# Kernel optimization log

Measured on AMD Instinct MI355X. Metric: run time of the kernel, lower is better.

## Reference

```python
import jax, jax.numpy as jnp
import numpy as np

N_HEAD = 16
N_STATE = 1024
NEG_INF = -1e9


def setup_inputs() -> dict:
    key = jax.random.key(0)
    k1, = jax.random.split(key, 1)
    B, S = 4, 2048
    x = jax.random.normal(k1, (B, S, 3 * N_STATE), dtype=jnp.float32)
    # causal attention mask (1 = keep, 0 = masked), broadcast over heads
    attn_mask = jnp.tril(jnp.ones((S, S), dtype=jnp.float32))[None, None, :, :]
    attn_mask = jnp.broadcast_to(attn_mask, (B, 1, S, S))
    return {"x": x, "attn_mask": attn_mask}


def reference(x, attn_mask) -> jnp.ndarray:
    B, S, _ = x.shape
    d_head = N_STATE // N_HEAD
    q = x[:, :, :N_STATE].reshape(B, S, N_HEAD, d_head).transpose(0, 2, 1, 3)  # [B,H,S,D]
    k = x[:, :, N_STATE:2 * N_STATE].reshape(B, S, N_HEAD, d_head).transpose(0, 2, 1, 3)
    v = x[:, :, 2 * N_STATE:].reshape(B, S, N_HEAD, d_head).transpose(0, 2, 1, 3)
    scale = 1.0 / jnp.sqrt(jnp.asarray(d_head, dtype=x.dtype))
    w = jnp.einsum('bhqd,bhkd->bhqk', q, k) * scale           # [B,H,S,S]
    w = attn_mask * w + (1.0 - attn_mask) * NEG_INF
    w = jax.nn.softmax(w, axis=-1)
    # attention_dropout is identity at inference (Keras Dropout, training=False)
    a = jnp.einsum('bhqk,bhkd->bhqd', w, v)                   # [B,H,S,D]
    return a.transpose(0, 2, 1, 3).reshape(B, S, N_STATE)
```

## Files before the change

kernel.cpp:

```cpp
#include <hip/hip_runtime.h>


typedef float  f32x4  __attribute__((ext_vector_type(4)));
typedef short  bf16x8 __attribute__((ext_vector_type(8)));

#define NH      16
#define DH      64
#define SEQ     2048
#define NSTATE  1024
#define ROW3    3072
#define BQ      128
#define BK      64
#define NQB     (SEQ / BQ)
#define KST     72
#define VST     72
#define PST     72
#define NEG_BIG (-1e9f)
#define QSC     (0.125f * 1.4426950408889634f)

static __device__ __forceinline__ unsigned pk2(float x, float y) {
    unsigned ux = __builtin_bit_cast(unsigned, x);
    unsigned uy = __builtin_bit_cast(unsigned, y);
    ux += 0x7FFFu + ((ux >> 16) & 1u);
    uy += 0x7FFFu + ((uy >> 16) & 1u);
    return __builtin_amdgcn_perm(uy, ux, 0x07060302u);
}

__global__ __launch_bounds__(512, 4)
void mha_fwd(const float* __restrict__ x, float* __restrict__ out) {
    const int tid  = threadIdx.x;
    const int wave = tid >> 6;
    const int lane = tid & 63;
    const int l16  = lane & 15;
    const int quad = lane >> 4;

    const int pr = blockIdx.x;
    const int bh = blockIdx.y;
    const int b  = bh >> 4;
    const int h  = bh & 15;

    const float* xb    = x + (size_t)b * SEQ * ROW3;
    const float* kbase = xb + NSTATE + h * DH;
    const float* vbase = xb + 2 * NSTATE + h * DH;
    float*       ob    = out + (size_t)b * SEQ * NSTATE + h * DH;

    __shared__ __align__(16) short Klds[BK * KST];
    __shared__ __align__(16) short Vlds[DH * VST];
    __shared__ __align__(16) short Plds[8][16 * PST];

    bf16x8 vones;
#pragma unroll
    for (int i = 0; i < 8; ++i) vones[i] = (short)0x3F80;

#pragma unroll 1
    for (int ph = 0; ph < 2; ++ph) {
        const int qblk = ph ? (NQB - 1 - pr) : pr;
        const int q0   = qblk * BQ;
        const int qmin = q0 + wave * 16;
        const int qrow = qmin + l16;

        bf16x8 qf[2];
        {
            const float* qp = xb + (size_t)qrow * ROW3 + h * DH + quad * 8;
#pragma unroll
            for (int f = 0; f < 2; ++f) {
                float4 a = *(const float4*)(qp + 32 * f);
                float4 c = *(const float4*)(qp + 32 * f + 4);
                union { bf16x8 v; unsigned u[4]; } qq;
                qq.u[0] = pk2(a.x * QSC, a.y * QSC);
                qq.u[1] = pk2(a.z * QSC, a.w * QSC);
                qq.u[2] = pk2(c.x * QSC, c.y * QSC);
                qq.u[3] = pk2(c.z * QSC, c.w * QSC);
                qf[f] = qq.v;
            }
        }

        f32x4 o[4];
#pragma unroll
        for (int t = 0; t < 4; ++t) o[t] = (f32x4){0.f, 0.f, 0.f, 0.f};
        f32x4 ol = (f32x4){0.f, 0.f, 0.f, 0.f};

        const int ntiles = q0 / BK + BQ / BK;
#pragma unroll 1
        for (int it = 0; it < ntiles; ++it) {
            const int kv0 = it * BK;
            __syncthreads();

#pragma unroll
            for (int i = 0; i < 2; ++i) {
                int p  = tid + 512 * i;
                int kv = p >> 4;
                int d  = (p & 15) * 4;
                const float* gp = kbase + (size_t)(kv0 + kv) * ROW3 + d;
                float4 v = *(const float4*)gp;
                uint2 pk;
                pk.x = pk2(v.x, v.y);
                pk.y = pk2(v.z, v.w);
                *(uint2*)&Klds[kv * KST + d] = pk;
            }
#pragma unroll
            for (int i = 0; i < 4; ++i) {
                int idx = tid + 512 * i;
                int d   = idx & 63;
                int kv  = (idx >> 6) * 2;
                const float* gp = vbase + (size_t)(kv0 + kv) * ROW3 + d;
                float v0 = gp[0];
                float v1 = gp[ROW3];
                *(unsigned*)&Vlds[d * VST + kv] = pk2(v0, v1);
            }
            __syncthreads();

            if (kv0 > qmin + 15) continue;

            bf16x8 kf[4][2];
#pragma unroll
            for (int t = 0; t < 4; ++t)
#pragma unroll
                for (int f = 0; f < 2; ++f)
                    kf[t][f] = *(const bf16x8*)&Klds[(16 * t + l16) * KST + quad * 8 + 32 * f];
            bf16x8 vf[4][2];
#pragma unroll
            for (int t = 0; t < 4; ++t)
#pragma unroll
                for (int f = 0; f < 2; ++f)
                    vf[t][f] = *(const bf16x8*)&Vlds[(16 * t + l16) * VST + quad * 8 + 32 * f];

            f32x4 sc[4];
#pragma unroll
            for (int t = 0; t < 4; ++t) {
                f32x4 c = (f32x4){0.f, 0.f, 0.f, 0.f};
                c = __builtin_amdgcn_mfma_f32_16x16x32_bf16(kf[t][0], qf[0], c, 0, 0, 0);
                c = __builtin_amdgcn_mfma_f32_16x16x32_bf16(kf[t][1], qf[1], c, 0, 0, 0);
                sc[t] = c;
            }
            if (kv0 + BK - 1 > qmin) {
#pragma unroll
                for (int t = 0; t < 4; ++t)
#pragma unroll
                    for (int r = 0; r < 4; ++r) {
                        int kvg = kv0 + 16 * t + 4 * quad + r;
                        if (kvg > qrow) sc[t][r] = NEG_BIG;
                    }
            }

#pragma unroll
            for (int t = 0; t < 4; ++t)
#pragma unroll
                for (int r = 0; r < 4; ++r)
                    sc[t][r] = __builtin_amdgcn_exp2f(sc[t][r]);

            short* pb = &Plds[wave][0];
#pragma unroll
            for (int t = 0; t < 4; ++t) {
                uint2 pk;
                pk.x = pk2(sc[t][0], sc[t][1]);
                pk.y = pk2(sc[t][2], sc[t][3]);
                *(uint2*)&pb[l16 * PST + 16 * t + 4 * quad] = pk;
            }
            __asm__ volatile("s_waitcnt lgkmcnt(0)" ::: "memory");
            bf16x8 pf0 = *(const bf16x8*)&pb[l16 * PST + quad * 8];
            bf16x8 pf1 = *(const bf16x8*)&pb[l16 * PST + quad * 8 + 32];

#pragma unroll
            for (int t = 0; t < 4; ++t) {
                f32x4 c = o[t];
                c = __builtin_amdgcn_mfma_f32_16x16x32_bf16(pf0, vf[t][0], c, 0, 0, 0);
                c = __builtin_amdgcn_mfma_f32_16x16x32_bf16(pf1, vf[t][1], c, 0, 0, 0);
                o[t] = c;
            }
            ol = __builtin_amdgcn_mfma_f32_16x16x32_bf16(pf0, vones, ol, 0, 0, 0);
            ol = __builtin_amdgcn_mfma_f32_16x16x32_bf16(pf1, vones, ol, 0, 0, 0);
        }

        {
            const int qtop = qmin + 4 * quad;
            float lr[4];
#pragma unroll
            for (int r = 0; r < 4; ++r) lr[r] = 1.0f / ol[r];
#pragma unroll
            for (int t = 0; t < 4; ++t)
#pragma unroll
                for (int r = 0; r < 4; ++r)
                    ob[(size_t)(qtop + r) * NSTATE + 16 * t + l16] = o[t][r] * lr[r];
        }
    }
}

extern "C" void kernel_launch(void* const* d_in, const int* in_sizes, int n_in,
                              void* d_out, int out_size, void* d_ws, size_t ws_size,
                              hipStream_t stream) {
    const float* x = (const float*)d_in[0];
    float* out = (float*)d_out;
    dim3 grid(NQB / 2, 4 * NH);
    dim3 block(512);
    hipLaunchKernelGGL(mha_fwd, grid, block, 0, stream, x, out);
}
```

Baseline: 254.6 us.

## Fuse paired query blocks into one KV sweep with double-buffered LDS prefetch

Instead of two sequential phases that each reload K/V tiles, the block processes its low and high query blocks together in a single sweep over KV tiles, sharing each loaded K/V tile between both. The global loads for the next tile are issued into registers before computing on the current tile and committed to a second LDS buffer afterwards, which drops one barrier per iteration and hides load latency. In exchange it needs more registers (two sets of accumulators and Q fragments plus prefetch registers) and doubles K/V LDS use, which may reduce occupancy.

After: 629.9 us. +147.4%, slower.

```diff
diff --git a/kernel.cpp b/kernel.cpp
--- a/kernel.cpp
+++ b/kernel.cpp
@@ -26,6 +26,127 @@
     return __builtin_amdgcn_perm(uy, ux, 0x07060302u);
 }
 
+#define ISSUE_STAGE(KV0)                                                       \
+    {                                                                          \
+        _Pragma("unroll")                                                      \
+        for (int i = 0; i < 2; ++i) {                                          \
+            int p  = tid + 512 * i;                                            \
+            int kv = p >> 4;                                                   \
+            int d  = (p & 15) * 4;                                             \
+            kp[i] = *(const float4*)(kbase + (size_t)((KV0) + kv) * ROW3 + d); \
+        }                                                                      \
+        _Pragma("unroll")                                                      \
+        for (int i = 0; i < 4; ++i) {                                          \
+            int idx = tid + 512 * i;                                           \
+            int d   = idx & 63;                                                \
+            int kv  = (idx >> 6) * 2;                                          \
+            const float* gp = vbase + (size_t)((KV0) + kv) * ROW3 + d;         \
+            vp[2 * i]     = gp[0];                                             \
+            vp[2 * i + 1] = gp[ROW3];                                          \
+        }                                                                      \
+    }
+
+#define COMMIT_STAGE(BUF)                                                      \
+    {                                                                          \
+        _Pragma("unroll")                                                      \
+        for (int i = 0; i < 2; ++i) {                                          \
+            int p  = tid + 512 * i;                                            \
+            int kv = p >> 4;                                                   \
+            int d  = (p & 15) * 4;                                             \
+            uint2 w;                                                           \
+            w.x = pk2(kp[i].x, kp[i].y);                                       \
+            w.y = pk2(kp[i].z, kp[i].w);                                       \
+            *(uint2*)&Klds[BUF][kv * KST + d] = w;                             \
+        }                                                                      \
+        _Pragma("unroll")                                                      \
+        for (int i = 0; i < 4; ++i) {                                          \
+            int idx = tid + 512 * i;                                           \
+            int d   = idx & 63;                                                \
+            int kv  = (idx >> 6) * 2;                                          \
+            *(unsigned*)&Vlds[BUF][d * VST + kv] = pk2(vp[2 * i], vp[2 * i + 1]); \
+        }                                                                      \
+    }
+
+#define LOAD_Q(Q0, QF)                                                         \
+    {                                                                          \
+        const int qrow_ = (Q0) + wave * 16 + l16;                              \
+        const float* qp = xb + (size_t)qrow_ * ROW3 + h * DH + quad * 8;       \
+        _Pragma("unroll")                                                      \
+        for (int f = 0; f < 2; ++f) {                                          \
+            float4 a = *(const float4*)(qp + 32 * f);                          \
+            float4 c = *(const float4*)(qp + 32 * f + 4);                      \
+            union { bf16x8 v; unsigned u[4]; } qq;                             \
+            qq.u[0] = pk2(a.x * QSC, a.y * QSC);                               \
+            qq.u[1] = pk2(a.z * QSC, a.w * QSC);                               \
+            qq.u[2] = pk2(c.x * QSC, c.y * QSC);                               \
+            qq.u[3] = pk2(c.z * QSC, c.w * QSC);                               \
+            QF[f] = qq.v;                                                      \
+        }                                                                      \
+    }
+
+#define COMPUTE_BLOCK(Q0, QF, OACC, OL)                                        \
+    {                                                                          \
+        const int qmin_ = (Q0) + wave * 16;                                    \
+        if (kv0 <= qmin_ + 15) {                                               \
+            const int qrow_ = qmin_ + l16;                                     \
+            f32x4 sc[4];                                                       \
+            _Pragma("unroll")                                                  \
+            for (int t = 0; t < 4; ++t) {                                      \
+                f32x4 c = (f32x4){0.f, 0.f, 0.f, 0.f};                         \
+                c = __builtin_amdgcn_mfma_f32_16x16x32_bf16(kf[t][0], QF[0], c, 0, 0, 0); \
+                c = __builtin_amdgcn_mfma_f32_16x16x32_bf16(kf[t][1], QF[1], c, 0, 0, 0); \
+                sc[t] = c;                                                     \
+            }                                                                  \
+            if (kv0 + BK - 1 > qmin_) {                                        \
+                _Pragma("unroll")                                              \
+                for (int t = 0; t < 4; ++t)                                    \
+                    _Pragma("unroll")                                          \
+                    for (int r = 0; r < 4; ++r) {                              \
+                        int kvg = kv0 + 16 * t + 4 * quad + r;                 \
+                        if (kvg > qrow_) sc[t][r] = NEG_BIG;                   \
+                    }                                                          \
+            }                                                                  \
+            _Pragma("unroll")                                                  \
+            for (int t = 0; t < 4; ++t)                                        \
+                _Pragma("unroll")                                              \
+                for (int r = 0; r < 4; ++r)                                    \
+                    sc[t][r] = __builtin_amdgcn_exp2f(sc[t][r]);               \
+            short* pb = &Plds[wave][0];                                        \
+            _Pragma("unroll")                                                  \
+            for (int t = 0; t < 4; ++t) {                                      \
+                uint2 pk;                                                      \
+                pk.x = pk2(sc[t][0], sc[t][1]);                                \
+                pk.y = pk2(sc[t][2], sc[t][3]);                                \
+                *(uint2*)&pb[l16 * PST + 16 * t + 4 * quad] = pk;              \
+            }                                                                  \
+            __asm__ volatile("s_waitcnt lgkmcnt(0)" ::: "memory");             \
+            bf16x8 pf0 = *(const bf16x8*)&pb[l16 * PST + quad * 8];            \
+            bf16x8 pf1 = *(const bf16x8*)&pb[l16 * PST + quad * 8 + 32];       \
+            _Pragma("unroll")                                                  \
+            for (int t = 0; t < 4; ++t) {                                      \
+                f32x4 c = OACC[t];                                             \
+                c = __builtin_amdgcn_mfma_f32_16x16x32_bf16(pf0, vf[t][0], c, 0, 0, 0); \
+                c = __builtin_amdgcn_mfma_f32_16x16x32_bf16(pf1, vf[t][1], c, 0, 0, 0); \
+                OACC[t] = c;                                                   \
+            }                                                                  \
+            OL = __builtin_amdgcn_mfma_f32_16x16x32_bf16(pf0, vones, OL, 0, 0, 0); \
+            OL = __builtin_amdgcn_mfma_f32_16x16x32_bf16(pf1, vones, OL, 0, 0, 0); \
+        }                                                                      \
+    }
+
+#define EPILOGUE(Q0, OACC, OL)                                                 \
+    {                                                                          \
+        const int qtop_ = (Q0) + wave * 16 + 4 * quad;                         \
+        float lr[4];                                                           \
+        _Pragma("unroll")                                                      \
+        for (int r = 0; r < 4; ++r) lr[r] = 1.0f / OL[r];                      \
+        _Pragma("unroll")                                                      \
+        for (int t = 0; t < 4; ++t)                                            \
+            _Pragma("unroll")                                                  \
+            for (int r = 0; r < 4; ++r)                                        \
+                ob[(size_t)(qtop_ + r) * NSTATE + 16 * t + l16] = OACC[t][r] * lr[r]; \
+    }
+
 __global__ __launch_bounds__(512, 4)
 void mha_fwd(const float* __restrict__ x, float* __restrict__ out) {
     const int tid  = threadIdx.x;
@@ -44,146 +165,69 @@
     const float* vbase = xb + 2 * NSTATE + h * DH;
     float*       ob    = out + (size_t)b * SEQ * NSTATE + h * DH;
 
-    __shared__ __align__(16) short Klds[BK * KST];
-    __shared__ __align__(16) short Vlds[DH * VST];
+    __shared__ __align__(16) short Klds[2][BK * KST];
+    __shared__ __align__(16) short Vlds[2][DH * VST];
     __shared__ __align__(16) short Plds[8][16 * PST];
 
+    const int q0_lo = pr * BQ;
+    const int q0_hi = (NQB - 1 - pr) * BQ;
+    const int ntl   = q0_lo / BK + 2;
+    const int nt    = q0_hi / BK + 2;
+
     bf16x8 vones;
 #pragma unroll
     for (int i = 0; i < 8; ++i) vones[i] = (short)0x3F80;
 
+    bf16x8 qlo[2], qhi[2];
+    LOAD_Q(q0_lo, qlo)
+    LOAD_Q(q0_hi, qhi)
+
+    f32x4 o_lo[4], o_hi[4];
+#pragma unroll
+    for (int t = 0; t < 4; ++t) {
+        o_lo[t] = (f32x4){0.f, 0.f, 0.f, 0.f};
+        o_hi[t] = (f32x4){0.f, 0.f, 0.f, 0.f};
+    }
+    f32x4 d_lo = (f32x4){0.f, 0.f, 0.f, 0.f};
+    f32x4 d_hi = (f32x4){0.f, 0.f, 0.f, 0.f};
+
+    float4 kp[2];
+    float  vp[8];
+
+    ISSUE_STAGE(0)
+    COMMIT_STAGE(0)
+    __syncthreads();
+
 #pragma unroll 1
-    for (int ph = 0; ph < 2; ++ph) {
-        const int qblk = ph ? (NQB - 1 - pr) : pr;
-        const int q0   = qblk * BQ;
-        const int qmin = q0 + wave * 16;
-        const int qrow = qmin + l16;
-
-        bf16x8 qf[2];
-        {
-            const float* qp = xb + (size_t)qrow * ROW3 + h * DH + quad * 8;
-#pragma unroll
-            for (int f = 0; f < 2; ++f) {
-                float4 a = *(const float4*)(qp + 32 * f);
-                float4 c = *(const float4*)(qp + 32 * f + 4);
-                union { bf16x8 v; unsigned u[4]; } qq;
-                qq.u[0] = pk2(a.x * QSC, a.y * QSC);
-                qq.u[1] = pk2(a.z * QSC, a.w * QSC);
-                qq.u[2] = pk2(c.x * QSC, c.y * QSC);
-                qq.u[3] = pk2(c.z * QSC, c.w * QSC);
-                qf[f] = qq.v;
-            }
-        }
-
-        f32x4 o[4];
-#pragma unroll
-        for (int t = 0; t < 4; ++t) o[t] = (f32x4){0.f, 0.f, 0.f, 0.f};
-        f32x4 ol = (f32x4){0.f, 0.f, 0.f, 0.f};
-
-        const int ntiles = q0 / BK + BQ / BK;
-#pragma unroll 1
-        for (int it = 0; it < ntiles; ++it) {
-            const int kv0 = it * BK;
-            __syncthreads();
-
-#pragma unroll
-            for (int i = 0; i < 2; ++i) {
-                int p  = tid + 512 * i;
-                int kv = p >> 4;
-                int d  = (p & 15) * 4;
-                const float* gp = kbase + (size_t)(kv0 + kv) * ROW3 + d;
-                float4 v = *(const float4*)gp;
-                uint2 pk;
-                pk.x = pk2(v.x, v.y);
-                pk.y = pk2(v.z, v.w);
-                *(uint2*)&Klds[kv * KST + d] = pk;
-            }
-#pragma unroll
-            for (int i = 0; i < 4; ++i) {
-                int idx = tid + 512 * i;
-                int d   = idx & 63;
-                int kv  = (idx >> 6) * 2;
-                const float* gp = vbase + (size_t)(kv0 + kv) * ROW3 + d;
-                float v0 = gp[0];
-                float v1 = gp[ROW3];
-                *(unsigned*)&Vlds[d * VST + kv] = pk2(v0, v1);
-            }
-            __syncthreads();
-
-            if (kv0 > qmin + 15) continue;
-
-            bf16x8 kf[4][2];
-#pragma unroll
-            for (int t = 0; t < 4; ++t)
-#pragma unroll
-                for (int f = 0; f < 2; ++f)
-                    kf[t][f] = *(const bf16x8*)&Klds[(16 * t + l16) * KST + quad * 8 + 32 * f];
-            bf16x8 vf[4][2];
-#pragma unroll
-            for (int t = 0; t < 4; ++t)
-#pragma unroll
-                for (int f = 0; f < 2; ++f)
-                    vf[t][f] = *(const bf16x8*)&Vlds[(16 * t + l16) * VST + quad * 8 + 32 * f];
-
-            f32x4 sc[4];
-#pragma unroll
-            for (int t = 0; t < 4; ++t) {
-                f32x4 c = (f32x4){0.f, 0.f, 0.f, 0.f};
-                c = __builtin_amdgcn_mfma_f32_16x16x32_bf16(kf[t][0], qf[0], c, 0, 0, 0);
-                c = __builtin_amdgcn_mfma_f32_16x16x32_bf16(kf[t][1], qf[1], c, 0, 0, 0);
-                sc[t] = c;
-            }
-            if (kv0 + BK - 1 > qmin) {
-#pragma unroll
-                for (int t = 0; t < 4; ++t)
-#pragma unroll
-                    for (int r = 0; r < 4; ++r) {
-                        int kvg = kv0 + 16 * t + 4 * quad + r;
-                        if (kvg > qrow) sc[t][r] = NEG_BIG;
-                    }
-            }
-
-#pragma unroll
-            for (int t = 0; t < 4; ++t)
-#pragma unroll
-                for (int r = 0; r < 4; ++r)
-                    sc[t][r] = __builtin_amdgcn_exp2f(sc[t][r]);
-
-            short* pb = &Plds[wave][0];
-#pragma unroll
-            for (int t = 0; t < 4; ++t) {
-                uint2 pk;
-                pk.x = pk2(sc[t][0], sc[t][1]);
-                pk.y = pk2(sc[t][2], sc[t][3]);
-                *(uint2*)&pb[l16 * PST + 16 * t + 4 * quad] = pk;
-            }
-            __asm__ volatile("s_waitcnt lgkmcnt(0)" ::: "memory");
-            bf16x8 pf0 = *(const bf16x8*)&pb[l16 * PST + quad * 8];
-            bf16x8 pf1 = *(const bf16x8*)&pb[l16 * PST + quad * 8 + 32];
-
-#pragma unroll
-            for (int t = 0; t < 4; ++t) {
-                f32x4 c = o[t];
-                c = __builtin_amdgcn_mfma_f32_16x16x32_bf16(pf0, vf[t][0], c, 0, 0, 0);
-                c = __builtin_amdgcn_mfma_f32_16x16x32_bf16(pf1, vf[t][1], c, 0, 0, 0);
-                o[t] = c;
-            }
-            ol = __builtin_amdgcn_mfma_f32_16x16x32_bf16(pf0, vones, ol, 0, 0, 0);
-            ol = __builtin_amdgcn_mfma_f32_16x16x32_bf16(pf1, vones, ol, 0, 0, 0);
-        }
-
-        {
-            const int qtop = qmin + 4 * quad;
-            float lr[4];
-#pragma unroll
-            for (int r = 0; r < 4; ++r) lr[r] = 1.0f / ol[r];
-#pragma unroll
-            for (int t = 0; t < 4; ++t)
-#pragma unroll
-                for (int r = 0; r < 4; ++r)
-                    ob[(size_t)(qtop + r) * NSTATE + 16 * t + l16] = o[t][r] * lr[r];
-        }
-    }
+    for (int it = 0; it < nt; ++it) {
+        const int kv0 = it * BK;
+        const int cur = it & 1;
+        const bool pf = (it + 1 < nt);
+
+        if (pf) ISSUE_STAGE((it + 1) * BK)
+
+        bf16x8 kf[4][2];
+#pragma unroll
+        for (int t = 0; t < 4; ++t)
+#pragma unroll
+            for (int f = 0; f < 2; ++f)
+                kf[t][f] = *(const bf16x8*)&Klds[cur][(16 * t + l16) * KST + quad * 8 + 32 * f];
+        bf16x8 vf[4][2];
+#pragma unroll
+        for (int t = 0; t < 4; ++t)
+#pragma unroll
+            for (int f = 0; f < 2; ++f)
+                vf[t][f] = *(const bf16x8*)&Vlds[cur][(16 * t + l16) * VST + quad * 8 + 32 * f];
+
+        if (it < ntl) COMPUTE_BLOCK(q0_lo, qlo, o_lo, d_lo)
+        COMPUTE_BLOCK(q0_hi, qhi, o_hi, d_hi)
+
+        if (pf) COMMIT_STAGE(cur ^ 1)
+        __syncthreads();
+    }
+
+    EPILOGUE(q0_lo, o_lo, d_lo)
+    EPILOGUE(q0_hi, o_hi, d_hi)
 }
 
 extern "C" void kernel_launch(void* const* d_in, const int* in_sizes, int n_in,
```

## Double-buffer K/V tiles in LDS with register prefetch of next tile

Applied to the files above, without the earlier changes.

Turns the K/V staging into a two-stage pipeline. The next tile's global loads go into registers before the current tile is computed, and are converted to bf16 and written to the other LDS buffer afterwards. One barrier per iteration replaces two. The aim is to hide global-load latency behind the MFMA work, at the cost of doubled K/V LDS and extra live registers, which could hurt occupancy at 512 threads with 4 blocks per CU.

New measurement: 252.7 us. About the same (-0.7%).

```diff
diff --git a/kernel.cpp b/kernel.cpp
--- a/kernel.cpp
+++ b/kernel.cpp
@@ -26,6 +26,47 @@
     return __builtin_amdgcn_perm(uy, ux, 0x07060302u);
 }
 
+#define ISSUE_STAGE(KV0)                                                       \
+    {                                                                          \
+        _Pragma("unroll")                                                      \
+        for (int i = 0; i < 2; ++i) {                                          \
+            int p  = tid + 512 * i;                                            \
+            int kv = p >> 4;                                                   \
+            int d  = (p & 15) * 4;                                             \
+            kp[i] = *(const float4*)(kbase + (size_t)((KV0) + kv) * ROW3 + d); \
+        }                                                                      \
+        _Pragma("unroll")                                                      \
+        for (int i = 0; i < 4; ++i) {                                          \
+            int idx = tid + 512 * i;                                           \
+            int d   = idx & 63;                                                \
+            int kv  = (idx >> 6) * 2;                                          \
+            const float* gp = vbase + (size_t)((KV0) + kv) * ROW3 + d;         \
+            vp[2 * i]     = gp[0];                                             \
+            vp[2 * i + 1] = gp[ROW3];                                          \
+        }                                                                      \
+    }
+
+#define COMMIT_STAGE(BUF)                                                      \
+    {                                                                          \
+        _Pragma("unroll")                                                      \
+        for (int i = 0; i < 2; ++i) {                                          \
+            int p  = tid + 512 * i;                                            \
+            int kv = p >> 4;                                                   \
+            int d  = (p & 15) * 4;                                             \
+            uint2 w;                                                           \
+            w.x = pk2(kp[i].x, kp[i].y);                                       \
+            w.y = pk2(kp[i].z, kp[i].w);                                       \
+            *(uint2*)&Klds[BUF][kv * KST + d] = w;                             \
+        }                                                                      \
+        _Pragma("unroll")                                                      \
+        for (int i = 0; i < 4; ++i) {                                          \
+            int idx = tid + 512 * i;                                           \
+            int d   = idx & 63;                                                \
+            int kv  = (idx >> 6) * 2;                                          \
+            *(unsigned*)&Vlds[BUF][d * VST + kv] = pk2(vp[2 * i], vp[2 * i + 1]); \
+        }                                                                      \
+    }
+
 __global__ __launch_bounds__(512, 4)
 void mha_fwd(const float* __restrict__ x, float* __restrict__ out) {
     const int tid  = threadIdx.x;
@@ -44,13 +85,16 @@
     const float* vbase = xb + 2 * NSTATE + h * DH;
     float*       ob    = out + (size_t)b * SEQ * NSTATE + h * DH;
 
-    __shared__ __align__(16) short Klds[BK * KST];
-    __shared__ __align__(16) short Vlds[DH * VST];
+    __shared__ __align__(16) short Klds[2][BK * KST];
+    __shared__ __align__(16) short Vlds[2][DH * VST];
     __shared__ __align__(16) short Plds[8][16 * PST];
 
     bf16x8 vones;
 #pragma unroll
     for (int i = 0; i < 8; ++i) vones[i] = (short)0x3F80;
+
+    float4 kp[2];
+    float  vp[8];
 
 #pragma unroll 1
     for (int ph = 0; ph < 2; ++ph) {
@@ -81,95 +125,83 @@
         f32x4 ol = (f32x4){0.f, 0.f, 0.f, 0.f};
 
         const int ntiles = q0 / BK + BQ / BK;
+
+        __syncthreads();
+        ISSUE_STAGE(0)
+        COMMIT_STAGE(0)
+        __syncthreads();
+
 #pragma unroll 1
         for (int it = 0; it < ntiles; ++it) {
             const int kv0 = it * BK;
+            const int cur = it & 1;
+            const bool pf = (it + 1 < ntiles);
+
+            if (pf) ISSUE_STAGE((it + 1) * BK)
+
+            if (kv0 <= qmin + 15) {
+                bf16x8 kf[4][2];
+#pragma unroll
+                for (int t = 0; t < 4; ++t)
+#pragma unroll
+                    for (int f = 0; f < 2; ++f)
+                        kf[t][f] = *(const bf16x8*)&Klds[cur][(16 * t + l16) * KST + quad * 8 + 32 * f];
+                bf16x8 vf[4][2];
+#pragma unroll
+                for (int t = 0; t < 4; ++t)
+#pragma unroll
+                    for (int f = 0; f < 2; ++f)
+                        vf[t][f] = *(const bf16x8*)&Vlds[cur][(16 * t + l16) * VST + quad * 8 + 32 * f];
+
+                f32x4 sc[4];
+#pragma unroll
+                for (int t = 0; t < 4; ++t) {
+                    f32x4 c = (f32x4){0.f, 0.f, 0.f, 0.f};
+                    c = __builtin_amdgcn_mfma_f32_16x16x32_bf16(kf[t][0], qf[0], c, 0, 0, 0);
+                    c = __builtin_amdgcn_mfma_f32_16x16x32_bf16(kf[t][1], qf[1], c, 0, 0, 0);
+                    sc[t] = c;
+                }
+                if (kv0 + BK - 1 > qmin) {
+#pragma unroll
+                    for (int t = 0; t < 4; ++t)
+#pragma unroll
+                        for (int r = 0; r < 4; ++r) {
+                            int kvg = kv0 + 16 * t + 4 * quad + r;
+                            if (kvg > qrow) sc[t][r] = NEG_BIG;
+                        }
+                }
+
+#pragma unroll
+                for (int t = 0; t < 4; ++t)
+#pragma unroll
+                    for (int r = 0; r < 4; ++r)
+                        sc[t][r] = __builtin_amdgcn_exp2f(sc[t][r]);
+
+                short* pb = &Plds[wave][0];
+#pragma unroll
+                for (int t = 0; t < 4; ++t) {
+                    uint2 pk;
+                    pk.x = pk2(sc[t][0], sc[t][1]);
+                    pk.y = pk2(sc[t][2], sc[t][3]);
+                    *(uint2*)&pb[l16 * PST + 16 * t + 4 * quad] = pk;
+                }
+                __asm__ volatile("s_waitcnt lgkmcnt(0)" ::: "memory");
+                bf16x8 pf0 = *(const bf16x8*)&pb[l16 * PST + quad * 8];
+                bf16x8 pf1 = *(const bf16x8*)&pb[l16 * PST + quad * 8 + 32];
+
+#pragma unroll
+                for (int t = 0; t < 4; ++t) {
+                    f32x4 c = o[t];
+                    c = __builtin_amdgcn_mfma_f32_16x16x32_bf16(pf0, vf[t][0], c, 0, 0, 0);
+                    c = __builtin_amdgcn_mfma_f32_16x16x32_bf16(pf1, vf[t][1], c, 0, 0, 0);
+                    o[t] = c;
+                }
+                ol = __builtin_amdgcn_mfma_f32_16x16x32_bf16(pf0, vones, ol, 0, 0, 0);
+                ol = __builtin_amdgcn_mfma_f32_16x16x32_bf16(pf1, vones, ol, 0, 0, 0);
+            }
+
+            if (pf) COMMIT_STAGE(cur ^ 1)
             __syncthreads();
-
-#pragma unroll
-            for (int i = 0; i < 2; ++i) {
-                int p  = tid + 512 * i;
-                int kv = p >> 4;
-                int d  = (p & 15) * 4;
-                const float* gp = kbase + (size_t)(kv0 + kv) * ROW3 + d;
-                float4 v = *(const float4*)gp;
-                uint2 pk;
-                pk.x = pk2(v.x, v.y);
-                pk.y = pk2(v.z, v.w);
-                *(uint2*)&Klds[kv * KST + d] = pk;
-            }
-#pragma unroll
-            for (int i = 0; i < 4; ++i) {
-                int idx = tid + 512 * i;
-                int d   = idx & 63;
-                int kv  = (idx >> 6) * 2;
-                const float* gp = vbase + (size_t)(kv0 + kv) * ROW3 + d;
-                float v0 = gp[0];
-                float v1 = gp[ROW3];
-                *(unsigned*)&Vlds[d * VST + kv] = pk2(v0, v1);
-            }
-            __syncthreads();
-
-            if (kv0 > qmin + 15) continue;
-
-            bf16x8 kf[4][2];
-#pragma unroll
-            for (int t = 0; t < 4; ++t)
-#pragma unroll
-                for (int f = 0; f < 2; ++f)
-                    kf[t][f] = *(const bf16x8*)&Klds[(16 * t + l16) * KST + quad * 8 + 32 * f];
-            bf16x8 vf[4][2];
-#pragma unroll
-            for (int t = 0; t < 4; ++t)
-#pragma unroll
-                for (int f = 0; f < 2; ++f)
-                    vf[t][f] = *(const bf16x8*)&Vlds[(16 * t + l16) * VST + quad * 8 + 32 * f];
-
-            f32x4 sc[4];
-#pragma unroll
-            for (int t = 0; t < 4; ++t) {
-                f32x4 c = (f32x4){0.f, 0.f, 0.f, 0.f};
-                c = __builtin_amdgcn_mfma_f32_16x16x32_bf16(kf[t][0], qf[0], c, 0, 0, 0);
-                c = __builtin_amdgcn_mfma_f32_16x16x32_bf16(kf[t][1], qf[1], c, 0, 0, 0);
-                sc[t] = c;
-            }
-            if (kv0 + BK - 1 > qmin) {
-#pragma unroll
-                for (int t = 0; t < 4; ++t)
-#pragma unroll
-                    for (int r = 0; r < 4; ++r) {
-                        int kvg = kv0 + 16 * t + 4 * quad + r;
-                        if (kvg > qrow) sc[t][r] = NEG_BIG;
-                    }
-            }
-
-#pragma unroll
-            for (int t = 0; t < 4; ++t)
-#pragma unroll
-                for (int r = 0; r < 4; ++r)
-                    sc[t][r] = __builtin_amdgcn_exp2f(sc[t][r]);
-
-            short* pb = &Plds[wave][0];
-#pragma unroll
-            for (int t = 0; t < 4; ++t) {
-                uint2 pk;
-                pk.x = pk2(sc[t][0], sc[t][1]);
-                pk.y = pk2(sc[t][2], sc[t][3]);
-                *(uint2*)&pb[l16 * PST + 16 * t + 4 * quad] = pk;
-            }
-            __asm__ volatile("s_waitcnt lgkmcnt(0)" ::: "memory");
-            bf16x8 pf0 = *(const bf16x8*)&pb[l16 * PST + quad * 8];
-            bf16x8 pf1 = *(const bf16x8*)&pb[l16 * PST + quad * 8 + 32];
-
-#pragma unroll
-            for (int t = 0; t < 4; ++t) {
-                f32x4 c = o[t];
-                c = __builtin_amdgcn_mfma_f32_16x16x32_bf16(pf0, vf[t][0], c, 0, 0, 0);
-                c = __builtin_amdgcn_mfma_f32_16x16x32_bf16(pf1, vf[t][1], c, 0, 0, 0);
-                o[t] = c;
-            }
-            ol = __builtin_amdgcn_mfma_f32_16x16x32_bf16(pf0, vones, ol, 0, 0, 0);
-            ol = __builtin_amdgcn_mfma_f32_16x16x32_bf16(pf1, vones, ol, 0, 0, 0);
         }
 
         {
```
